# Performance work log

Measured on AMD Instinct MI355X. Metric: run time of the kernel, lower is better.

The kernel has to match this reference:

```python
import jax, jax.numpy as jnp
import numpy as np

ALPHA_ENT = 1.1          # entmax alpha used at call site (default arg)
N_ITER = 50              # entmax_bisect default iteration count
B, N, DIM = 256, 200, 128


def _entmax_bisect_raw(X, alpha=ALPHA_ENT, n_iter=N_ITER):
    # Faithful port of entmax_bisect (Peters & Martins): bisection on the
    # threshold tau s.t. sum_j max((alpha-1)x_j - tau, 0)^(1/(alpha-1)) = 1.
    d = X.shape[-1]
    Xs = X * (alpha - 1.0)
    max_val = jnp.max(Xs, axis=-1, keepdims=True)
    inv = 1.0 / (alpha - 1.0)

    def p_of(tau):
        return jnp.maximum(Xs - tau, 0.0) ** inv

    tau_lo = max_val - 1.0                      # 1 ** (alpha-1)
    tau_hi = max_val - (1.0 / d) ** (alpha - 1.0)
    f_lo = jnp.sum(p_of(tau_lo), axis=-1, keepdims=True) - 1.0
    dm0 = tau_hi - tau_lo

    def body(carry, _):
        tau_lo, dm = carry
        dm = dm * 0.5
        tau_m = tau_lo + dm
        f_m = jnp.sum(p_of(tau_m), axis=-1, keepdims=True) - 1.0
        tau_lo = jnp.where(f_m * f_lo >= 0, tau_m, tau_lo)
        return (tau_lo, dm), None

    (tau_lo, _), _ = jax.lax.scan(body, (tau_lo, dm0), None, length=n_iter)
    p = p_of(tau_lo)
    return p / jnp.sum(p, axis=-1, keepdims=True)   # ensure_sum_one=True


@jax.custom_vjp
def entmax_bisect(X):
    return _entmax_bisect_raw(X)


def _entmax_fwd(X):
    Y = _entmax_bisect_raw(X)
    return Y, Y


def _entmax_bwd(Y, dY):
    # analytic entmax backward: dX = dY*gppr - (sum(dY*gppr)/sum(gppr))*gppr
    gppr = jnp.where(Y > 0, Y ** (2.0 - ALPHA_ENT), 0.0)
    dX = dY * gppr
    q = jnp.sum(dX, axis=-1, keepdims=True) / jnp.sum(gppr, axis=-1, keepdims=True)
    return (dX - q * gppr,)


entmax_bisect.defvjp(_entmax_fwd, _entmax_bwd)


def setup_inputs() -> dict:
    key = jax.random.key(0)
    ks = jax.random.split(key, 8)
    hidden = jax.random.normal(ks[0], (B, N, DIM), dtype=jnp.float32)
    adj = jax.random.randint(ks[1], (B, N, N), 0, 5, dtype=jnp.int64)  # edge types 0..4
    mask = jax.random.randint(ks[2], (B, N), 0, 2, dtype=jnp.int64)
    mask = mask.at[:, 0].set(1)  # guarantee no fully-masked row
    scale = 1.0 / np.sqrt(DIM)
    a0 = jax.random.normal(ks[3], (DIM, 1), dtype=jnp.float32) * scale
    a1 = jax.random.normal(ks[4], (DIM, 1), dtype=jnp.float32) * scale
    a2 = jax.random.normal(ks[5], (DIM, 1), dtype=jnp.float32) * scale
    a3 = jax.random.normal(ks[6], (DIM, 1), dtype=jnp.float32) * scale
    kw, kb = jax.random.split(ks[7])
    W = jax.random.normal(kw, (2 * DIM, DIM), dtype=jnp.float32) * (1.0 / np.sqrt(2 * DIM))
    b = jax.random.normal(kb, (DIM,), dtype=jnp.float32) * 0.01
    return {"hidden": hidden, "adj": adj, "mask": mask,
            "a0": a0, "a1": a1, "a2": a2, "a3": a3, "W": W, "b": b}


def reference(hidden, adj, mask, a0, a1, a2, a3, W, b):
    # e_k[b,i,j] = leakyrelu( sum_d h[b,i,d]*h[b,j,d]*a_k[d] )  -- fuses the
    # original [B,N*N,dim] a_input materialization into one contraction.
    A = jnp.concatenate([a0, a1, a2, a3], axis=-1)            # [dim, 4]
    e = jnp.einsum('bid,bjd,dk->kbij', hidden, hidden, A)      # [4,B,N,N]
    e = jax.nn.leaky_relu(e, negative_slope=0.2)
    sel = jnp.zeros_like(e[0])
    sel = jnp.where(adj == 1, e[0], sel)
    sel = jnp.where(adj == 2, e[1], sel)
    sel = jnp.where(adj == 3, e[2], sel)
    sel = jnp.where(adj == 4, e[3], sel)
    sel = jnp.where(mask[:, None, :] == 0, -jnp.inf, sel)     # mask_ fill
    p = entmax_bisect(sel)                                     # [B,N,N]
    # dropout is identity in eval mode
    output = jnp.einsum('bij,bjd->bid', p, hidden)             # [B,N,dim]
    gate = jax.nn.sigmoid(jnp.concatenate([hidden, output], axis=-1) @ W + b)
    return gate * output + (1.0 - gate) * hidden
```

## Files before the change

### kernel.cpp

```cpp
#include <hip/hip_runtime.h>
#include <math.h>

#define NB    200
#define DIMH  128
#define TPB8  512
#define ROWS8 8
#define NITER 12
#define NJT   13
#define KJ2   112

typedef __attribute__((ext_vector_type(8))) short  short8v;
typedef __attribute__((ext_vector_type(4))) float  f32x4;
typedef __attribute__((ext_vector_type(4))) unsigned u32x4;

#define WF_U32 32768

__device__ __forceinline__ unsigned pack_hi2(float a, float b){
    return (__builtin_bit_cast(unsigned, a) >> 16) |
           (__builtin_bit_cast(unsigned, b) & 0xFFFF0000u);
}
__device__ __forceinline__ float hi_of(float x){
    return __builtin_bit_cast(float, __builtin_bit_cast(unsigned, x) & 0xFFFF0000u);
}
__device__ __forceinline__ float rdlane(float v, int l){
    return __builtin_bit_cast(float,
        __builtin_amdgcn_readlane(__builtin_bit_cast(int, v), l));
}
__device__ __forceinline__ float wsum_dpp(float v){
#define DPP_ADD(ctrl, rmask)                                                     \
    {                                                                            \
        int t_ = __builtin_amdgcn_update_dpp(0, __builtin_bit_cast(int, v),      \
                                             ctrl, rmask, 0xf, false);           \
        v += __builtin_bit_cast(float, t_);                                      \
    }
    DPP_ADD(0x111, 0xf)
    DPP_ADD(0x112, 0xf)
    DPP_ADD(0x114, 0xf)
    DPP_ADD(0x118, 0xf)
    DPP_ADD(0x142, 0xa)
    DPP_ADD(0x143, 0xc)
#undef DPP_ADD
    return rdlane(v, 63);
}
__device__ __forceinline__ float wmax_dpp(float v){
#define DPP_MAX(ctrl, rmask)                                                     \
    {                                                                            \
        int t_ = __builtin_amdgcn_update_dpp(__builtin_bit_cast(int, v),         \
                                             __builtin_bit_cast(int, v),         \
                                             ctrl, rmask, 0xf, false);           \
        v = fmaxf(v, __builtin_bit_cast(float, t_));                             \
    }
    DPP_MAX(0x111, 0xf)
    DPP_MAX(0x112, 0xf)
    DPP_MAX(0x114, 0xf)
    DPP_MAX(0x118, 0xf)
    DPP_MAX(0x142, 0xa)
    DPP_MAX(0x143, 0xc)
#undef DPP_MAX
    return rdlane(v, 63);
}

__global__ __launch_bounds__(64) void conv_w(const float* __restrict__ W,
                                             unsigned* __restrict__ wf){
    const int lane = threadIdx.x;
    const int ks = blockIdx.x & 7, nt = blockIdx.x >> 3;
    const int krow = ks * 32 + (lane >> 4) * 8;
    const int col  = nt * 16 + (lane & 15);
    unsigned hi[4], lo[4];
    #pragma unroll
    for (int q2 = 0; q2 < 4; ++q2) {
        float v0 = W[(size_t)(krow + 2 * q2) * DIMH + col];
        float v1 = W[(size_t)(krow + 2 * q2 + 1) * DIMH + col];
        hi[q2] = pack_hi2(v0, v1);
        lo[q2] = pack_hi2(v0 - hi_of(v0), v1 - hi_of(v1));
    }
    const unsigned base = (blockIdx.x * 64 + lane) * 4;
    *(u32x4*)&wf[base]              = (u32x4){hi[0], hi[1], hi[2], hi[3]};
    *(u32x4*)&wf[WF_U32 / 2 + base] = (u32x4){lo[0], lo[1], lo[2], lo[3]};
}

__global__ __launch_bounds__(256) void conv_hs(const float* __restrict__ hidden,
                                               unsigned* __restrict__ hs_hi,
                                               unsigned* __restrict__ hs_lo){
    size_t gid = (size_t)blockIdx.x * 256 + threadIdx.x;
    float2 h2 = *(const float2*)(hidden + gid * 2);
    hs_hi[gid] = pack_hi2(h2.x, h2.y);
    hs_lo[gid] = pack_hi2(h2.x - hi_of(h2.x), h2.y - hi_of(h2.y));
}

__global__ __launch_bounds__(256) void conv_ht(const float* __restrict__ hidden,
                                               unsigned* __restrict__ ht_hi){
    __shared__ float tile[32][33];
    const int bid = blockIdx.x;
    const int b  = bid / 28;
    const int rem = bid % 28;
    const int jt = rem >> 2, dt = rem & 3;
    const int j0 = jt * 32, d0 = dt * 32;
    const int tt = threadIdx.x;
    #pragma unroll
    for (int rr = 0; rr < 4; ++rr) {
        int j = j0 + (tt >> 5) + rr * 8;
        int d = d0 + (tt & 31);
        tile[(tt >> 5) + rr * 8][tt & 31] =
            (j < NB) ? hidden[((size_t)b * NB + j) * DIMH + d] : 0.0f;
    }
    __syncthreads();
    #pragma unroll
    for (int it = 0; it < 2; ++it) {
        int j2 = it * 8 + (tt & 7);
        int dl = tt >> 3;
        float v0 = tile[2 * j2][dl];
        float v1 = tile[2 * j2 + 1][dl];
        size_t o = ((size_t)b * DIMH + d0 + dl) * KJ2 + (j0 >> 1) + j2;
        ht_hi[o] = pack_hi2(v0, v1);
    }
}

__global__ __launch_bounds__(TPB8, 4) void la_fused8(
    const float* __restrict__ hidden,
    const int*   __restrict__ adj,
    const int*   __restrict__ mask,
    const float* __restrict__ a0, const float* __restrict__ a1,
    const float* __restrict__ a2, const float* __restrict__ a3,
    const float* __restrict__ bias,
    const unsigned* __restrict__ wf,
    const unsigned* __restrict__ hs_hi, const unsigned* __restrict__ hs_lo,
    const unsigned* __restrict__ ht_hi,
    float* __restrict__ out)
{
    __shared__ unsigned hab[2][32][68];
    __shared__ float xs[ROWS8][208];
    __shared__ float cop[ROWS8][256];
    __shared__ unsigned pbf[2 * ROWS8 * 116];
    __shared__ unsigned cbf[2][ROWS8][132];

    const int t    = threadIdx.x;
    const int lane = t & 63;
    const int r    = t >> 6;
    const int d2   = 2 * lane;
    const int bid  = (blockIdx.x & 7) * ((int)gridDim.x >> 3) + (blockIdx.x >> 3);
    const int b    = bid / (NB / ROWS8);
    const int i0   = (bid % (NB / ROWS8)) * ROWS8;

    const float* hb = hidden + (size_t)b * NB * DIMH;

    for (int idx = t; idx < ROWS8 * DIMH; idx += TPB8) {
        int rr = idx >> 7, d = idx & 127;
        cop[rr][d] = hb[(i0 + rr) * DIMH + d];
    }
    for (int s = t; s < 32 * 64; s += TPB8) {
        int rk = s >> 6, dd = s & 63;
        int rr = rk >> 2, k = rk & 3;
        int d  = dd * 2;
        const float* ap = (k == 0) ? a0 : (k == 1) ? a1 : (k == 2) ? a2 : a3;
        float h0 = hb[(i0 + rr) * DIMH + d];
        float h1 = hb[(i0 + rr) * DIMH + d + 1];
        float q0 = h0 * ap[d];
        float q1 = h1 * ap[d + 1];
        hab[0][rk][dd] = pack_hi2(q0, q1);
        hab[1][rk][dd] = pack_hi2(q0 - hi_of(q0), q1 - hi_of(q1));
    }
    __syncthreads();

    short8v Ahi[2][4], Alo[2][4];
    {
        const int au = (lane >> 4) * 4;
        #pragma unroll
        for (int tl = 0; tl < 2; ++tl) {
            const int arow = tl * 16 + (lane & 15);
            #pragma unroll
            for (int ks = 0; ks < 4; ++ks) {
                Ahi[tl][ks] = __builtin_bit_cast(short8v, *(const u32x4*)&hab[0][arow][ks * 16 + au]);
                Alo[tl][ks] = __builtin_bit_cast(short8v, *(const u32x4*)&hab[1][arow][ks * 16 + au]);
            }
        }
    }

    const int jcol = lane & 15;
    const int kgrp = lane >> 4;
    for (int jt = r; jt < NJT; jt += 8) {
        const int jrow = jt * 16 + jcol;
        const int jl   = (jrow < NB) ? jrow : (NB - 1);
        f32x4 acc0 = {0.f, 0.f, 0.f, 0.f};
        f32x4 acc1 = {0.f, 0.f, 0.f, 0.f};
        const unsigned* bhp = hs_hi + ((size_t)(b * NB + jl) << 6) + kgrp * 4;
        const unsigned* blp = hs_lo + ((size_t)(b * NB + jl) << 6) + kgrp * 4;
        #pragma unroll
        for (int ks = 0; ks < 4; ++ks) {
            short8v Bh = __builtin_bit_cast(short8v, *(const u32x4*)(bhp + ks * 16));
            short8v Bl = __builtin_bit_cast(short8v, *(const u32x4*)(blp + ks * 16));
            acc0 = __builtin_amdgcn_mfma_f32_16x16x32_bf16(Ahi[0][ks], Bh, acc0, 0, 0, 0);
            acc0 = __builtin_amdgcn_mfma_f32_16x16x32_bf16(Alo[0][ks], Bh, acc0, 0, 0, 0);
            acc0 = __builtin_amdgcn_mfma_f32_16x16x32_bf16(Ahi[0][ks], Bl, acc0, 0, 0, 0);
            acc1 = __builtin_amdgcn_mfma_f32_16x16x32_bf16(Ahi[1][ks], Bh, acc1, 0, 0, 0);
            acc1 = __builtin_amdgcn_mfma_f32_16x16x32_bf16(Alo[1][ks], Bh, acc1, 0, 0, 0);
            acc1 = __builtin_amdgcn_mfma_f32_16x16x32_bf16(Ahi[1][ks], Bl, acc1, 0, 0, 0);
        }
        const int mm  = mask[b * NB + jl];
        const int kk0 = adj[(size_t)(b * NB + i0 + kgrp) * NB + jl];
        const int kk1 = adj[(size_t)(b * NB + i0 + 4 + kgrp) * NB + jl];
        float ev0 = (kk0 == 1) ? acc0[0] : (kk0 == 2) ? acc0[1] :
                    (kk0 == 3) ? acc0[2] : (kk0 == 4) ? acc0[3] : 0.0f;
        float ev1 = (kk1 == 1) ? acc1[0] : (kk1 == 2) ? acc1[1] :
                    (kk1 == 3) ? acc1[2] : (kk1 == 4) ? acc1[3] : 0.0f;
        ev0 = (ev0 >= 0.0f) ? ev0 : 0.2f * ev0;
        ev1 = (ev1 >= 0.0f) ? ev1 : 0.2f * ev1;
        float xv0 = ev0 * 0.1f;
        float xv1 = ev1 * 0.1f;
        if (mm == 0 || jrow >= NB) { xv0 = -INFINITY; xv1 = -INFINITY; }
        xs[kgrp][jrow]     = xv0;
        xs[4 + kgrp][jrow] = xv1;
    }
    __syncthreads();

    float x0 = xs[r][lane];
    float x1 = xs[r][lane + 64];
    float x2 = xs[r][lane + 128];
    float x3 = (lane < 16) ? xs[r][192 + lane] : -INFINITY;

    float mx  = wmax_dpp(fmaxf(fmaxf(x0, x1), fmaxf(x2, x3)));
    float tau = mx - 1.0f;
    #define P10(v, tt) ({ float z_ = fmaxf((v) - (tt), 0.f); float z2 = z_*z_; float z4 = z2*z2; float z8 = z4*z4; z8*z2; })
    float s0 = P10(x0, tau) + P10(x1, tau) + P10(x2, tau) + P10(x3, tau);
    float f_lo = wsum_dpp(s0) - 1.0f;
    float dm   = (mx - 0.58870401f) - tau;

    for (int itn = 0; itn < NITER; ++itn) {
        dm *= 0.5f;
        float tm = tau + dm;
        float s = P10(x0, tm) + P10(x1, tm) + P10(x2, tm) + P10(x3, tm);
        float fm = wsum_dpp(s) - 1.0f;
        if (fm * f_lo >= 0.0f) tau = tm;
    }
    float p0 = P10(x0, tau);
    float p1 = P10(x1, tau);
    float p2 = P10(x2, tau);
    float p3 = P10(x3, tau);
    #undef P10
    float sinv = 1.0f / wsum_dpp(p0 + p1 + p2 + p3);
    xs[r][lane]       = p0 * sinv;
    xs[r][lane + 64]  = p1 * sinv;
    xs[r][lane + 128] = p2 * sinv;
    if (lane < 16) xs[r][192 + lane] = p3 * sinv;

    for (int k2 = lane; k2 < KJ2; k2 += 64) {
        int j = 2 * k2;
        float v0 = (j < 208)     ? xs[r][j]     : 0.0f;
        float v1 = (j + 1 < 208) ? xs[r][j + 1] : 0.0f;
        pbf[r * 116 + k2]                = pack_hi2(v0, v1);
        pbf[ROWS8 * 116 + r * 116 + k2]  = pack_hi2(v0 - hi_of(v0), v1 - hi_of(v1));
    }
    __syncthreads();

    {
        f32x4 av = {0.f, 0.f, 0.f, 0.f};
        const int prow = lane & 7;
        const int au   = (lane >> 4) * 4;
        const int dc   = 16 * r + (lane & 15);
        const size_t base = ((size_t)(b * DIMH + dc)) * KJ2 + au;
        #pragma unroll
        for (int ks = 0; ks < 7; ++ks) {
            short8v Ph = __builtin_bit_cast(short8v, *(const u32x4*)&pbf[prow * 116 + ks * 16 + au]);
            short8v Pl = __builtin_bit_cast(short8v, *(const u32x4*)&pbf[ROWS8 * 116 + prow * 116 + ks * 16 + au]);
            short8v Bh = __builtin_bit_cast(short8v, *(const u32x4*)(ht_hi + base + ks * 16));
            av = __builtin_amdgcn_mfma_f32_16x16x32_bf16(Ph, Bh, av, 0, 0, 0);
            av = __builtin_amdgcn_mfma_f32_16x16x32_bf16(Pl, Bh, av, 0, 0, 0);
        }
        if (lane < 32) {
            const int rbase = (lane >> 4) * 4;
            #pragma unroll
            for (int q = 0; q < 4; ++q)
                cop[rbase + q][DIMH + 16 * r + (lane & 15)] = av[q];
        }
    }
    __syncthreads();

    float2 ovv = *(const float2*)&cop[r][DIMH + d2];

    {
        float hx = cop[r][d2], hy = cop[r][d2 + 1];
        cbf[0][r][lane]      = pack_hi2(hx, hy);
        cbf[1][r][lane]      = pack_hi2(hx - hi_of(hx), hy - hi_of(hy));
        cbf[0][r][64 + lane] = pack_hi2(ovv.x, ovv.y);
        cbf[1][r][64 + lane] = pack_hi2(ovv.x - hi_of(ovv.x), ovv.y - hi_of(ovv.y));
    }
    __syncthreads();

    {
        f32x4 ga = {0.f, 0.f, 0.f, 0.f};
        const int arow = lane & 7;
        const int au   = (lane >> 4) * 4;
        #pragma unroll
        for (int ks = 0; ks < 8; ++ks) {
            short8v Ah = __builtin_bit_cast(short8v, *(const u32x4*)&cbf[0][arow][ks * 16 + au]);
            short8v Al = __builtin_bit_cast(short8v, *(const u32x4*)&cbf[1][arow][ks * 16 + au]);
            const unsigned bi = ((r * 8 + ks) * 64 + lane) * 4;
            short8v Bh = __builtin_bit_cast(short8v, *(const u32x4*)&wf[bi]);
            ga = __builtin_amdgcn_mfma_f32_16x16x32_bf16(Ah, Bh, ga, 0, 0, 0);
            ga = __builtin_amdgcn_mfma_f32_16x16x32_bf16(Al, Bh, ga, 0, 0, 0);
        }
        if (lane < 32) {
            const int rbase = (lane >> 4) * 4;
            #pragma unroll
            for (int q = 0; q < 4; ++q)
                xs[rbase + q][16 * r + (lane & 15)] = ga[q];
        }
    }
    __syncthreads();

    {
        float2 bv = *(const float2*)(bias + d2);
        float gx = xs[r][d2]     + bv.x;
        float gy = xs[r][d2 + 1] + bv.y;
        float sgx = 1.0f / (1.0f + __expf(-gx));
        float sgy = 1.0f / (1.0f + __expf(-gy));
        float2 hf = *(const float2*)&cop[r][d2];
        const size_t gi = (size_t)(b * NB + i0 + r) * DIMH;
        float2 res;
        res.x = sgx * ovv.x + (1.0f - sgx) * hf.x;
        res.y = sgy * ovv.y + (1.0f - sgy) * hf.y;
        *(float2*)(out + gi + d2) = res;
    }
}

#define ROWS  4
#define TPB   256
template<int MODE>
__global__ __launch_bounds__(TPB, 4) void la_fused(
    const float* __restrict__ hidden,
    const int*   __restrict__ adj,
    const int*   __restrict__ mask,
    const float* __restrict__ a0, const float* __restrict__ a1,
    const float* __restrict__ a2, const float* __restrict__ a3,
    const float* __restrict__ W,  const float* __restrict__ bias,
    const unsigned* __restrict__ wf,
    float* __restrict__ out)
{
    __shared__ unsigned hab[2][16][68];
    __shared__ float xs[ROWS][208];
    __shared__ float cop[ROWS][256];
    __shared__ float scrf[ROWS * ROWS * DIMH];
    __shared__ unsigned cbf[2][ROWS][132];

    const int t    = threadIdx.x;
    const int lane = t & 63;
    const int r    = t >> 6;
    const int d2   = 2 * lane;
    const int bid  = blockIdx.x;
    const int b    = bid / (NB / ROWS);
    const int i0   = (bid % (NB / ROWS)) * ROWS;

    const float* hb = hidden + (size_t)b * NB * DIMH;

    for (int idx = t; idx < ROWS * DIMH; idx += TPB) {
        int rr = idx >> 7, d = idx & 127;
        cop[rr][d] = hb[(i0 + rr) * DIMH + d];
    }
    for (int s = t; s < 16 * 64; s += TPB) {
        int rk = s >> 6, dd = s & 63;
        int rr = rk >> 2, k = rk & 3;
        int d  = dd * 2;
        const float* ap = (k == 0) ? a0 : (k == 1) ? a1 : (k == 2) ? a2 : a3;
        float h0 = hb[(i0 + rr) * DIMH + d];
        float h1 = hb[(i0 + rr) * DIMH + d + 1];
        float q0 = h0 * ap[d];
        float q1 = h1 * ap[d + 1];
        hab[0][rk][dd] = pack_hi2(q0, q1);
        hab[1][rk][dd] = pack_hi2(q0 - hi_of(q0), q1 - hi_of(q1));
    }
    __syncthreads();

    short8v Ahi[4], Alo[4];
    {
        const int arow = lane & 15;
        const int au   = (lane >> 4) * 4;
        #pragma unroll
        for (int ks = 0; ks < 4; ++ks) {
            Ahi[ks] = __builtin_bit_cast(short8v, *(const u32x4*)&hab[0][arow][ks * 16 + au]);
            Alo[ks] = __builtin_bit_cast(short8v, *(const u32x4*)&hab[1][arow][ks * 16 + au]);
        }
    }

    const int jcol = lane & 15;
    const int kgrp = lane >> 4;
    for (int jt = r; jt < NJT; jt += 4) {
        const int jrow = jt * 16 + jcol;
        const int jl   = (jrow < NB) ? jrow : (NB - 1);
        const float* hj = hb + (size_t)jl * DIMH + kgrp * 8;
        f32x4 acc = {0.f, 0.f, 0.f, 0.f};
        #pragma unroll
        for (int ks = 0; ks < 4; ++ks) {
            float4 ra = *(const float4*)(hj + ks * 32);
            float4 rb = *(const float4*)(hj + ks * 32 + 4);
            u32x4 bh = { pack_hi2(ra.x, ra.y), pack_hi2(ra.z, ra.w),
                         pack_hi2(rb.x, rb.y), pack_hi2(rb.z, rb.w) };
            u32x4 bl = { pack_hi2(ra.x - hi_of(ra.x), ra.y - hi_of(ra.y)),
                         pack_hi2(ra.z - hi_of(ra.z), ra.w - hi_of(ra.w)),
                         pack_hi2(rb.x - hi_of(rb.x), rb.y - hi_of(rb.y)),
                         pack_hi2(rb.z - hi_of(rb.z), rb.w - hi_of(rb.w)) };
            short8v Bh = __builtin_bit_cast(short8v, bh);
            short8v Bl = __builtin_bit_cast(short8v, bl);
            acc = __builtin_amdgcn_mfma_f32_16x16x32_bf16(Ahi[ks], Bh, acc, 0, 0, 0);
            acc = __builtin_amdgcn_mfma_f32_16x16x32_bf16(Alo[ks], Bh, acc, 0, 0, 0);
            acc = __builtin_amdgcn_mfma_f32_16x16x32_bf16(Ahi[ks], Bl, acc, 0, 0, 0);
        }
        int kk = adj[(size_t)(b * NB + i0 + kgrp) * NB + jl];
        int mm = mask[b * NB + jl];
        float ev = (kk == 1) ? acc[0] : (kk == 2) ? acc[1] :
                   (kk == 3) ? acc[2] : (kk == 4) ? acc[3] : 0.0f;
        ev = (ev >= 0.0f) ? ev : 0.2f * ev;
        float x = ev * 0.1f;
        if (mm == 0)     x = -INFINITY;
        if (jrow >= NB)  x = -INFINITY;
        xs[kgrp][jrow] = x;
    }
    __syncthreads();

    float x0 = xs[r][lane];
    float x1 = xs[r][lane + 64];
    float x2 = xs[r][lane + 128];
    float x3 = (lane < 16) ? xs[r][192 + lane] : -INFINITY;

    float mx  = wmax_dpp(fmaxf(fmaxf(x0, x1), fmaxf(x2, x3)));
    float tau = mx - 1.0f;
    #define P10(v, tt) ({ float z_ = fmaxf((v) - (tt), 0.f); float z2 = z_*z_; float z4 = z2*z2; float z8 = z4*z4; z8*z2; })
    float s0 = P10(x0, tau) + P10(x1, tau) + P10(x2, tau) + P10(x3, tau);
    float f_lo = wsum_dpp(s0) - 1.0f;
    float dm   = (mx - 0.58870401f) - tau;

    for (int itn = 0; itn < NITER; ++itn) {
        dm *= 0.5f;
        float tm = tau + dm;
        float s = P10(x0, tm) + P10(x1, tm) + P10(x2, tm) + P10(x3, tm);
        float fm = wsum_dpp(s) - 1.0f;
        if (fm * f_lo >= 0.0f) tau = tm;
    }
    float p0 = P10(x0, tau);
    float p1 = P10(x1, tau);
    float p2 = P10(x2, tau);
    float p3 = P10(x3, tau);
    #undef P10
    float sinv = 1.0f / wsum_dpp(p0 + p1 + p2 + p3);
    xs[r][lane]       = p0 * sinv;
    xs[r][lane + 64]  = p1 * sinv;
    xs[r][lane + 128] = p2 * sinv;
    if (lane < 16) xs[r][192 + lane] = p3 * sinv;
    __syncthreads();

    const int J0 = r * 50;
    float pj0 = (lane < 50) ? xs[0][J0 + lane] : 0.f;
    float pj1 = (lane < 50) ? xs[1][J0 + lane] : 0.f;
    float pj2 = (lane < 50) ? xs[2][J0 + lane] : 0.f;
    float pj3 = (lane < 50) ? xs[3][J0 + lane] : 0.f;
    float2 ov0 = {0.f,0.f}, ov1 = {0.f,0.f}, ov2 = {0.f,0.f}, ov3 = {0.f,0.f};
    {
        const float* hjb = hb + (size_t)J0 * DIMH + d2;
        #pragma unroll 5
        for (int jj = 0; jj < 50; ++jj) {
            float2 hv = *(const float2*)(hjb + jj * DIMH);
            float c0 = rdlane(pj0, jj), c1 = rdlane(pj1, jj);
            float c2 = rdlane(pj2, jj), c3 = rdlane(pj3, jj);
            ov0.x = fmaf(c0, hv.x, ov0.x); ov0.y = fmaf(c0, hv.y, ov0.y);
            ov1.x = fmaf(c1, hv.x, ov1.x); ov1.y = fmaf(c1, hv.y, ov1.y);
            ov2.x = fmaf(c2, hv.x, ov2.x); ov2.y = fmaf(c2, hv.y, ov2.y);
            ov3.x = fmaf(c3, hv.x, ov3.x); ov3.y = fmaf(c3, hv.y, ov3.y);
        }
    }
    *(float2*)&scrf[(r * 4 + 0) * DIMH + d2] = ov0;
    *(float2*)&scrf[(r * 4 + 1) * DIMH + d2] = ov1;
    *(float2*)&scrf[(r * 4 + 2) * DIMH + d2] = ov2;
    *(float2*)&scrf[(r * 4 + 3) * DIMH + d2] = ov3;
    __syncthreads();
    float2 o;
    {
        float2 q0 = *(const float2*)&scrf[(0 * 4 + r) * DIMH + d2];
        float2 q1 = *(const float2*)&scrf[(1 * 4 + r) * DIMH + d2];
        float2 q2 = *(const float2*)&scrf[(2 * 4 + r) * DIMH + d2];
        float2 q3 = *(const float2*)&scrf[(3 * 4 + r) * DIMH + d2];
        o.x = (q0.x + q1.x) + (q2.x + q3.x);
        o.y = (q0.y + q1.y) + (q2.y + q3.y);
    }
    *(float2*)&cop[r][DIMH + d2] = o;
    __syncthreads();

    float2 ov = *(const float2*)&cop[r][DIMH + d2];
    float2 gres;

    if constexpr (MODE >= 1) {
        float hx = cop[r][d2], hy = cop[r][d2 + 1];
        cbf[0][r][lane]      = pack_hi2(hx, hy);
        cbf[1][r][lane]      = pack_hi2(hx - hi_of(hx), hy - hi_of(hy));
        cbf[0][r][64 + lane] = pack_hi2(ov.x, ov.y);
        cbf[1][r][64 + lane] = pack_hi2(ov.x - hi_of(ov.x), ov.y - hi_of(ov.y));
        __syncthreads();
        f32x4 ga0 = {0.f,0.f,0.f,0.f}, ga1 = {0.f,0.f,0.f,0.f};
        const int arow = lane & 3;
        const int au   = (lane >> 4) * 4;
        #pragma unroll
        for (int ks = 0; ks < 8; ++ks) {
            short8v Ah = __builtin_bit_cast(short8v, *(const u32x4*)&cbf[0][arow][ks * 16 + au]);
            short8v Al = __builtin_bit_cast(short8v, *(const u32x4*)&cbf[1][arow][ks * 16 + au]);
            const unsigned bi0 = (((2 * r) * 8 + ks) * 64 + lane) * 4;
            const unsigned bi1 = (((2 * r + 1) * 8 + ks) * 64 + lane) * 4;
            short8v Bh0 = __builtin_bit_cast(short8v, *(const u32x4*)&wf[bi0]);
            short8v Bl0 = __builtin_bit_cast(short8v, *(const u32x4*)&wf[WF_U32 / 2 + bi0]);
            short8v Bh1 = __builtin_bit_cast(short8v, *(const u32x4*)&wf[bi1]);
            short8v Bl1 = __builtin_bit_cast(short8v, *(const u32x4*)&wf[WF_U32 / 2 + bi1]);
            ga0 = __builtin_amdgcn_mfma_f32_16x16x32_bf16(Ah, Bh0, ga0, 0, 0, 0);
            ga0 = __builtin_amdgcn_mfma_f32_16x16x32_bf16(Al, Bh0, ga0, 0, 0, 0);
            ga0 = __builtin_amdgcn_mfma_f32_16x16x32_bf16(Ah, Bl0, ga0, 0, 0, 0);
            ga1 = __builtin_amdgcn_mfma_f32_16x16x32_bf16(Ah, Bh1, ga1, 0, 0, 0);
            ga1 = __builtin_amdgcn_mfma_f32_16x16x32_bf16(Al, Bh1, ga1, 0, 0, 0);
            ga1 = __builtin_amdgcn_mfma_f32_16x16x32_bf16(Ah, Bl1, ga1, 0, 0, 0);
        }
        if (lane < 16) {
            #pragma unroll
            for (int m = 0; m < 4; ++m) {
                xs[m][(2 * r) * 16 + lane]     = ga0[m];
                xs[m][(2 * r + 1) * 16 + lane] = ga1[m];
            }
        }
        __syncthreads();
        gres.x = xs[r][d2];
        gres.y = xs[r][d2 + 1];
    } else {
        float cv0 = cop[0][64 * r + lane];
        float cv1 = cop[1][64 * r + lane];
        float cv2 = cop[2][64 * r + lane];
        float cv3 = cop[3][64 * r + lane];
        float2 gv0 = {0.f,0.f}, gv1 = {0.f,0.f}, gv2 = {0.f,0.f}, gv3 = {0.f,0.f};
        const float* wb = W + (size_t)(64 * r) * DIMH + d2;
        #pragma unroll 8
        for (int ee = 0; ee < 64; ++ee) {
            float2 wv = *(const float2*)(wb + ee * DIMH);
            float c0 = rdlane(cv0, ee), c1 = rdlane(cv1, ee);
            float c2 = rdlane(cv2, ee), c3 = rdlane(cv3, ee);
            gv0.x = fmaf(c0, wv.x, gv0.x); gv0.y = fmaf(c0, wv.y, gv0.y);
            gv1.x = fmaf(c1, wv.x, gv1.x); gv1.y = fmaf(c1, wv.y, gv1.y);
            gv2.x = fmaf(c2, wv.x, gv2.x); gv2.y = fmaf(c2, wv.y, gv2.y);
            gv3.x = fmaf(c3, wv.x, gv3.x); gv3.y = fmaf(c3, wv.y, gv3.y);
        }
        *(float2*)&scrf[(r * 4 + 0) * DIMH + d2] = gv0;
        *(float2*)&scrf[(r * 4 + 1) * DIMH + d2] = gv1;
        *(float2*)&scrf[(r * 4 + 2) * DIMH + d2] = gv2;
        *(float2*)&scrf[(r * 4 + 3) * DIMH + d2] = gv3;
        __syncthreads();
        float2 q0 = *(const float2*)&scrf[(0 * 4 + r) * DIMH + d2];
        float2 q1 = *(const float2*)&scrf[(1 * 4 + r) * DIMH + d2];
        float2 q2 = *(const float2*)&scrf[(2 * 4 + r) * DIMH + d2];
        float2 q3 = *(const float2*)&scrf[(3 * 4 + r) * DIMH + d2];
        gres.x = (q0.x + q1.x) + (q2.x + q3.x);
        gres.y = (q0.y + q1.y) + (q2.y + q3.y);
    }

    {
        float2 bv = *(const float2*)(bias + d2);
        float gx = gres.x + bv.x;
        float gy = gres.y + bv.y;
        float sgx = 1.0f / (1.0f + __expf(-gx));
        float sgy = 1.0f / (1.0f + __expf(-gy));
        float2 hf = *(const float2*)&cop[r][d2];
        const size_t gi = (size_t)(b * NB + i0 + r) * DIMH;
        float2 res;
        res.x = sgx * ov.x + (1.0f - sgx) * hf.x;
        res.y = sgy * ov.y + (1.0f - sgy) * hf.y;
        *(float2*)(out + gi + d2) = res;
    }
}

extern "C" void kernel_launch(void* const* d_in, const int* in_sizes, int n_in,
                              void* d_out, int out_size, void* d_ws, size_t ws_size,
                              hipStream_t stream)
{
    const float* hidden = (const float*)d_in[0];
    const int*   adj    = (const int*)d_in[1];
    const int*   mask   = (const int*)d_in[2];
    const float* a0     = (const float*)d_in[3];
    const float* a1     = (const float*)d_in[4];
    const float* a2     = (const float*)d_in[5];
    const float* a3     = (const float*)d_in[6];
    const float* W      = (const float*)d_in[7];
    const float* bias   = (const float*)d_in[8];
    float* out = (float*)d_out;

    const int B = in_sizes[0] / (NB * DIMH);

    const size_t hsN = (size_t)B * NB * 64;
    const size_t htN = (size_t)B * DIMH * KJ2;
    const size_t fullU32 = (size_t)WF_U32 + 2 * hsN + 2 * htN;

    if (ws_size >= fullU32 * sizeof(unsigned)) {
        unsigned* wf    = (unsigned*)d_ws;
        unsigned* hs_hi = wf + WF_U32;
        unsigned* hs_lo = hs_hi + hsN;
        unsigned* ht_hi = hs_lo + hsN;
        conv_w<<<64, 64, 0, stream>>>(W, wf);
        conv_hs<<<(unsigned)(hsN / 256), 256, 0, stream>>>(hidden, hs_hi, hs_lo);
        conv_ht<<<B * 28, 256, 0, stream>>>(hidden, ht_hi);
        dim3 grid8(B * (NB / ROWS8));
        la_fused8<<<grid8, TPB8, 0, stream>>>(hidden, adj, mask, a0, a1, a2, a3,
                                              bias, wf, hs_hi, hs_lo, ht_hi, out);
    } else if (ws_size >= (size_t)WF_U32 * sizeof(unsigned)) {
        unsigned* wf = (unsigned*)d_ws;
        conv_w<<<64, 64, 0, stream>>>(W, wf);
        dim3 grid4(B * (NB / ROWS));
        la_fused<1><<<grid4, TPB, 0, stream>>>(hidden, adj, mask, a0, a1, a2, a3,
                                               W, bias, wf, out);
    } else {
        dim3 grid4(B * (NB / ROWS));
        la_fused<0><<<grid4, TPB, 0, stream>>>(hidden, adj, mask, a0, a1, a2, a3,
                                               W, bias, nullptr, out);
    }
}
```

Before: 200.7 us.

## Replace entmax bisection with Newton iterations on a transformed root equation

Swaps the 12-step bisection for the entmax threshold for 6 Newton-style steps. Each step computes two moments (sum z^10 and sum z^9) with a paired DPP wave reduction, then updates tau in closed form using log2/exp2 and fast reciprocals. This roughly halves the number of serial wave reductions and power evaluations per row. It also widens the padding of several shared-memory arrays and aligns them to 16 bytes, likely to allow vector LDS access or avoid bank conflicts. The risk is accuracy: Newton convergence from tau = max - 1 and the approximate rcp could shift tau compared with bisection.

Measured after the change: 205.8 us. 2.5% more time.

```diff
diff --git a/kernel.cpp b/kernel.cpp
--- a/kernel.cpp
+++ b/kernel.cpp
@@ -6,6 +6,7 @@
 #define TPB8  512
 #define ROWS8 8
 #define NITER 12
+#define NNEWT 6
 #define NJT   13
 #define KJ2   112
 
@@ -41,6 +42,26 @@
     DPP_ADD(0x143, 0xc)
 #undef DPP_ADD
     return rdlane(v, 63);
+}
+__device__ __forceinline__ void wsum2_dpp(float& a, float& b){
+#define DPP2(ctrl, rmask)                                                        \
+    {                                                                            \
+        int ta = __builtin_amdgcn_update_dpp(0, __builtin_bit_cast(int, a),      \
+                                             ctrl, rmask, 0xf, false);           \
+        int tb = __builtin_amdgcn_update_dpp(0, __builtin_bit_cast(int, b),      \
+                                             ctrl, rmask, 0xf, false);           \
+        a += __builtin_bit_cast(float, ta);                                      \
+        b += __builtin_bit_cast(float, tb);                                      \
+    }
+    DPP2(0x111, 0xf)
+    DPP2(0x112, 0xf)
+    DPP2(0x114, 0xf)
+    DPP2(0x118, 0xf)
+    DPP2(0x142, 0xa)
+    DPP2(0x143, 0xc)
+#undef DPP2
+    a = rdlane(a, 63);
+    b = rdlane(b, 63);
 }
 __device__ __forceinline__ float wmax_dpp(float v){
 #define DPP_MAX(ctrl, rmask)                                                     \
@@ -128,11 +149,11 @@
     const unsigned* __restrict__ ht_hi,
     float* __restrict__ out)
 {
-    __shared__ unsigned hab[2][32][68];
+    __shared__ __align__(16) unsigned hab[2][32][84];
     __shared__ float xs[ROWS8][208];
     __shared__ float cop[ROWS8][256];
-    __shared__ unsigned pbf[2 * ROWS8 * 116];
-    __shared__ unsigned cbf[2][ROWS8][132];
+    __shared__ __align__(16) unsigned pbf[2 * ROWS8 * 116];
+    __shared__ __align__(16) unsigned cbf[2][ROWS8][148];
 
     const int t    = threadIdx.x;
     const int lane = t & 63;
@@ -220,18 +241,19 @@
 
     float mx  = wmax_dpp(fmaxf(fmaxf(x0, x1), fmaxf(x2, x3)));
     float tau = mx - 1.0f;
+    #pragma unroll
+    for (int itn = 0; itn < NNEWT; ++itn) {
+        float t10 = 0.f, t9 = 0.f;
+        #define ACC(xv) { float z_ = fmaxf((xv) - tau, 0.f); float e2 = z_*z_;   \
+                          float e8 = e2*e2; e8 = e8*e8; float e9 = e8*z_;        \
+                          t9 += e9; t10 = fmaf(e9, z_, t10); }
+        ACC(x0) ACC(x1) ACC(x2) ACC(x3)
+        #undef ACC
+        wsum2_dpp(t10, t9);
+        float u  = exp2f(0.1f * log2f(t10));
+        tau += t10 * (1.0f - __builtin_amdgcn_rcpf(u)) * __builtin_amdgcn_rcpf(t9);
+    }
     #define P10(v, tt) ({ float z_ = fmaxf((v) - (tt), 0.f); float z2 = z_*z_; float z4 = z2*z2; float z8 = z4*z4; z8*z2; })
-    float s0 = P10(x0, tau) + P10(x1, tau) + P10(x2, tau) + P10(x3, tau);
-    float f_lo = wsum_dpp(s0) - 1.0f;
-    float dm   = (mx - 0.58870401f) - tau;
-
-    for (int itn = 0; itn < NITER; ++itn) {
-        dm *= 0.5f;
-        float tm = tau + dm;
-        float s = P10(x0, tm) + P10(x1, tm) + P10(x2, tm) + P10(x3, tm);
-        float fm = wsum_dpp(s) - 1.0f;
-        if (fm * f_lo >= 0.0f) tau = tm;
-    }
     float p0 = P10(x0, tau);
     float p1 = P10(x1, tau);
     float p2 = P10(x2, tau);
```
